# Performance work log

Measured on AMD Instinct MI355X. Metric: run time of the kernel, lower is better.

The kernel has to match this reference:

```python
import jax, jax.numpy as jnp
import numpy as np

B, S, D_MODEL, H, D_K, D_V = 2, 2048, 1024, 16, 64, 64


def setup_inputs() -> dict:
    key = jax.random.key(0)
    ks = jax.random.split(key, 12)
    s = 0.02
    inp = {
        "Q": jax.random.normal(ks[0], (B, S, D_MODEL), jnp.float32),
        "K": jax.random.normal(ks[1], (B, S, D_MODEL), jnp.float32),
        "V": jax.random.normal(ks[2], (B, S, D_MODEL), jnp.float32),
        # causal 0/1 mask, broadcastable to [B, H, S, S]
        "mask": jnp.tril(jnp.ones((S, S), jnp.int32))[None, None, :, :],
        "Wq": jax.random.normal(ks[3], (D_MODEL, H * D_K), jnp.float32) * s,
        "bq": jnp.zeros((H * D_K,), jnp.float32),
        "Wk": jax.random.normal(ks[4], (D_MODEL, H * D_K), jnp.float32) * s,
        "bk": jnp.zeros((H * D_K,), jnp.float32),
        "Wv": jax.random.normal(ks[5], (D_MODEL, H * D_V), jnp.float32) * s,
        "bv": jnp.zeros((H * D_V,), jnp.float32),
        "Wo": jax.random.normal(ks[6], (H * D_V, D_MODEL), jnp.float32) * s,
        "bo": jnp.zeros((D_MODEL,), jnp.float32),
    }
    return inp


def reference(Q, K, V, mask, Wq, bq, Wk, bk, Wv, bv, Wo, bo):
    b = Q.shape[0]
    # project and split heads: [B, S, H*dk] -> [B, H, S, dk]
    q = (Q @ Wq + bq).reshape(b, -1, H, D_K).transpose(0, 2, 1, 3)
    k = (K @ Wk + bk).reshape(b, -1, H, D_K).transpose(0, 2, 1, 3)
    v = (V @ Wv + bv).reshape(b, -1, H, D_V).transpose(0, 2, 1, 3)
    scale = 1.0 / np.sqrt(D_K).astype(np.float32)
    scores = jnp.einsum("bhqd,bhkd->bhqk", q, k) * scale
    scores = jnp.where(mask == 0, jnp.float32(-1e9), scores)
    attn = jax.nn.softmax(scores, axis=-1)
    context = jnp.einsum("bhqk,bhkd->bhqd", attn, v)
    context = context.transpose(0, 2, 1, 3).reshape(b, -1, H * D_V)
    output = context @ Wo + bo  # dropout is identity in eval
    return output, attn
```

## Files before the change

### kernel.cpp

```cpp
#include <hip/hip_runtime.h>
#include <math.h>

#define S_LEN 2048
#define DMODEL 1024
#define NHEAD 16
#define HD 64
#define NBATCH 2

using short8  = __attribute__((ext_vector_type(8))) short;
using ushort8 = __attribute__((ext_vector_type(8))) unsigned short;
using floatx4 = __attribute__((ext_vector_type(4))) float;

__device__ __forceinline__ unsigned short f2b(float f) {
    unsigned int u = __float_as_uint(f);
    unsigned int r = (u + 0x7FFFu + ((u >> 16) & 1u)) >> 16;
    return (unsigned short)r;
}
__device__ __forceinline__ unsigned short f2bf(float f) {
    return (unsigned short)((__float_as_uint(f) + 0x8000u) >> 16);
}
__device__ __forceinline__ float b2f(unsigned short b) {
    return __uint_as_float(((unsigned int)b) << 16);
}

__device__ __forceinline__ void gll16(const void* g, void* l) {
    __builtin_amdgcn_global_load_lds(
        (const __attribute__((address_space(1))) unsigned int*)g,
        (__attribute__((address_space(3))) unsigned int*)l, 16, 0, 0);
}

#define C2_SCALE 0.18033688011112042f

__global__ __launch_bounds__(256)
void convert_bf16(const float* __restrict__ S0, const float* __restrict__ S1,
                  const float* __restrict__ S2,
                  unsigned short* __restrict__ D0, unsigned short* __restrict__ D1,
                  unsigned short* __restrict__ D2, int n4)
{
    const float* src = (blockIdx.z == 0) ? S0 : (blockIdx.z == 1) ? S1 : S2;
    unsigned short* dst = (blockIdx.z == 0) ? D0 : (blockIdx.z == 1) ? D1 : D2;
    int i = blockIdx.x * 256 + threadIdx.x;
    if (i < n4) {
        float4 v = ((const float4*)src)[i];
        ushort4 o;
        o.x = f2b(v.x); o.y = f2b(v.y); o.z = f2b(v.z); o.w = f2b(v.w);
        ((ushort4*)dst)[i] = o;
    }
}

__global__ __launch_bounds__(256)
void transpose_w(const float* __restrict__ W0, const float* __restrict__ W1,
                 const float* __restrict__ W2, const float* __restrict__ W3,
                 unsigned short* __restrict__ T0, unsigned short* __restrict__ T1,
                 unsigned short* __restrict__ T2, unsigned short* __restrict__ T3,
                 const float* __restrict__ bq, float* __restrict__ bqs)
{
    __shared__ float t[64][65];
    const float* W; unsigned short* T;
    switch (blockIdx.z) {
        case 0: W = W0; T = T0; break;
        case 1: W = W1; T = T1; break;
        case 2: W = W2; T = T2; break;
        default: W = W3; T = T3; break;
    }
    const int tid = threadIdx.x;
    const int c0 = blockIdx.x * 64;
    const int r0 = blockIdx.y * 64;

    if (blockIdx.z == 0 && blockIdx.x == 0 && blockIdx.y == 0) {
        float4 b4 = *(const float4*)(bq + tid * 4);
        b4.x *= C2_SCALE; b4.y *= C2_SCALE; b4.z *= C2_SCALE; b4.w *= C2_SCALE;
        *(float4*)(bqs + tid * 4) = b4;
    }

    const float scl = (blockIdx.z == 0) ? C2_SCALE : 1.0f;

    #pragma unroll
    for (int i = 0; i < 4; ++i) {
        int c = tid + i * 256;
        int r = c >> 4, off = (c & 15) * 4;
        float4 v = *(const float4*)(W + (size_t)(r0 + r) * DMODEL + c0 + off);
        t[r][off + 0] = v.x; t[r][off + 1] = v.y;
        t[r][off + 2] = v.z; t[r][off + 3] = v.w;
    }
    __syncthreads();
    #pragma unroll
    for (int i = 0; i < 4; ++i) {
        int c = tid + i * 256;
        int n = c >> 4, off = (c & 15) * 4;
        ushort4 o;
        o.x = f2b(t[off + 0][n] * scl); o.y = f2b(t[off + 1][n] * scl);
        o.z = f2b(t[off + 2][n] * scl); o.w = f2b(t[off + 3][n] * scl);
        *(ushort4*)(T + (size_t)(c0 + n) * DMODEL + r0 + off) = o;
    }
}

__global__ __launch_bounds__(256)
void gemm_qkv(const unsigned short* __restrict__ X0, const unsigned short* __restrict__ X1,
              const unsigned short* __restrict__ X2,
              const unsigned short* __restrict__ W0, const unsigned short* __restrict__ W1,
              const unsigned short* __restrict__ W2,
              const float* __restrict__ b0, const float* __restrict__ b1,
              const float* __restrict__ b2,
              unsigned short* __restrict__ o0, unsigned short* __restrict__ o1,
              unsigned short* __restrict__ o2)
{
    __shared__ unsigned short Xs[128 * 64];
    __shared__ unsigned short Ws[128 * 64];

    const unsigned short* X  = (blockIdx.z == 0) ? X0 : (blockIdx.z == 1) ? X1 : X2;
    const unsigned short* Wt = (blockIdx.z == 0) ? W0 : (blockIdx.z == 1) ? W1 : W2;
    const float* bias        = (blockIdx.z == 0) ? b0 : (blockIdx.z == 1) ? b1 : b2;
    unsigned short* outp     = (blockIdx.z == 0) ? o0 : (blockIdx.z == 1) ? o1 : o2;

    const int tid = threadIdx.x;
    const int lane = tid & 63, w = tid >> 6;
    const int l15 = lane & 15, l4 = lane >> 4;
    const int wr = w >> 1, wc = w & 1;
    const int row0 = blockIdx.y * 128;
    const int col0 = blockIdx.x * 128;

    const int srow = lane >> 3;
    const int sblk = (lane & 7) ^ srow;

    floatx4 acc[4][4] = {};

    for (int k0 = 0; k0 < DMODEL; k0 += 64) {
        __syncthreads();
        #pragma unroll
        for (int i = 0; i < 4; ++i)
            gll16(X + (size_t)(row0 + w * 32 + i * 8 + srow) * DMODEL + k0 + sblk * 8,
                  &Xs[(w * 32 + i * 8) * 64]);
        #pragma unroll
        for (int i = 0; i < 4; ++i)
            gll16(Wt + (size_t)(col0 + w * 32 + i * 8 + srow) * DMODEL + k0 + sblk * 8,
                  &Ws[(w * 32 + i * 8) * 64]);
        asm volatile("s_waitcnt vmcnt(0)" ::: "memory");
        __syncthreads();

        #pragma unroll
        for (int ks = 0; ks < 2; ++ks) {
            short8 a[4], b[4];
            #pragma unroll
            for (int m = 0; m < 4; ++m) {
                const int r = wr * 64 + m * 16 + l15;
                a[m] = *(const short8*)&Xs[r * 64 + (((ks * 4 + l4) ^ (r & 7)) << 3)];
            }
            #pragma unroll
            for (int n = 0; n < 4; ++n) {
                const int r = wc * 64 + n * 16 + l15;
                b[n] = *(const short8*)&Ws[r * 64 + (((ks * 4 + l4) ^ (r & 7)) << 3)];
            }
            #pragma unroll
            for (int m = 0; m < 4; ++m)
                #pragma unroll
                for (int n = 0; n < 4; ++n)
                    acc[m][n] = __builtin_amdgcn_mfma_f32_16x16x32_bf16(
                        a[m], b[n], acc[m][n], 0, 0, 0);
        }
    }

    float bl[4];
    #pragma unroll
    for (int n = 0; n < 4; ++n)
        bl[n] = bias[col0 + wc * 64 + n * 16 + l15];

    if (blockIdx.z != 2) {
        #pragma unroll
        for (int m = 0; m < 4; ++m)
            #pragma unroll
            for (int n = 0; n < 4; ++n) {
                const int gc = col0 + wc * 64 + n * 16 + l15;
                const int h = gc >> 6, d = gc & 63;
                #pragma unroll
                for (int reg = 0; reg < 4; ++reg) {
                    const int gr = row0 + wr * 64 + m * 16 + l4 * 4 + reg;
                    const int bb = gr >> 11, s = gr & 2047;
                    outp[(((size_t)bb * NHEAD + h) * S_LEN + s) * HD + d] =
                        f2b(acc[m][n][reg] + bl[n]);
                }
            }
    } else {
        #pragma unroll
        for (int m = 0; m < 4; ++m)
            #pragma unroll
            for (int n = 0; n < 4; ++n) {
                const int gc = col0 + wc * 64 + n * 16 + l15;
                const int h = gc >> 6, d = gc & 63;
                const int s0 = row0 + wr * 64 + m * 16 + l4 * 4;
                const int bb = s0 >> 11, sr = s0 & 2047;
                ushort4 pk;
                pk.x = f2b(acc[m][n][0] + bl[n]);
                pk.y = f2b(acc[m][n][1] + bl[n]);
                pk.z = f2b(acc[m][n][2] + bl[n]);
                pk.w = f2b(acc[m][n][3] + bl[n]);
                *(ushort4*)(outp + (((size_t)bb * NHEAD + h) * HD + d) * S_LEN + sr) = pk;
            }
    }
}

__global__ __launch_bounds__(256)
void gemm_out(const unsigned short* __restrict__ X, const unsigned short* __restrict__ Wt,
              const float* __restrict__ bias, float* __restrict__ out)
{
    __shared__ unsigned short Xs[128 * 64];
    __shared__ unsigned short Ws[64 * 64];

    const int tid = threadIdx.x;
    const int lane = tid & 63, w = tid >> 6;
    const int l15 = lane & 15, l4 = lane >> 4;
    const int wr = w >> 1, wc = w & 1;
    const int row0 = blockIdx.y * 128;
    const int col0 = blockIdx.x * 64;

    const int srow = lane >> 3;
    const int sblk = (lane & 7) ^ srow;

    floatx4 acc[4][2] = {};

    for (int k0 = 0; k0 < DMODEL; k0 += 64) {
        __syncthreads();
        #pragma unroll
        for (int i = 0; i < 4; ++i)
            gll16(X + (size_t)(row0 + w * 32 + i * 8 + srow) * DMODEL + k0 + sblk * 8,
                  &Xs[(w * 32 + i * 8) * 64]);
        #pragma unroll
        for (int i = 0; i < 2; ++i)
            gll16(Wt + (size_t)(col0 + w * 16 + i * 8 + srow) * DMODEL + k0 + sblk * 8,
                  &Ws[(w * 16 + i * 8) * 64]);
        asm volatile("s_waitcnt vmcnt(0)" ::: "memory");
        __syncthreads();

        #pragma unroll
        for (int ks = 0; ks < 2; ++ks) {
            short8 a[4], b[2];
            #pragma unroll
            for (int m = 0; m < 4; ++m) {
                const int r = wr * 64 + m * 16 + l15;
                a[m] = *(const short8*)&Xs[r * 64 + (((ks * 4 + l4) ^ (r & 7)) << 3)];
            }
            #pragma unroll
            for (int n = 0; n < 2; ++n) {
                const int r = wc * 32 + n * 16 + l15;
                b[n] = *(const short8*)&Ws[r * 64 + (((ks * 4 + l4) ^ (r & 7)) << 3)];
            }
            #pragma unroll
            for (int m = 0; m < 4; ++m)
                #pragma unroll
                for (int n = 0; n < 2; ++n)
                    acc[m][n] = __builtin_amdgcn_mfma_f32_16x16x32_bf16(
                        a[m], b[n], acc[m][n], 0, 0, 0);
        }
    }

    float bl[2];
    #pragma unroll
    for (int n = 0; n < 2; ++n)
        bl[n] = bias[col0 + wc * 32 + n * 16 + l15];

    #pragma unroll
    for (int m = 0; m < 4; ++m)
        #pragma unroll
        for (int n = 0; n < 2; ++n) {
            const int gc = col0 + wc * 32 + n * 16 + l15;
            #pragma unroll
            for (int reg = 0; reg < 4; ++reg) {
                const int gr = row0 + wr * 64 + m * 16 + l4 * 4 + reg;
                out[(size_t)gr * DMODEL + gc] = acc[m][n][reg] + bl[n];
            }
        }
}

__global__ __launch_bounds__(256)
void attn_mfma(const unsigned short* __restrict__ qg, const unsigned short* __restrict__ kg,
               const unsigned short* __restrict__ vtg, float* __restrict__ attn,
               unsigned short* __restrict__ ctx)
{
    __shared__ unsigned short Ks[2 * 64 * 64];
    __shared__ unsigned short Vt[64 * 64];
    __shared__ unsigned short Ps[64 * 88];

    const int tid = threadIdx.x;
    const int lane = tid & 63, w = tid >> 6;
    const int l15 = lane & 15, l4 = lane >> 4;

    const int i0 = blockIdx.x;
    const int local = i0 >> 3;
    const int bh = (i0 & 7) * 4 + (local & 3);
    const int qx = local >> 2;
    const int qb = (bh & 1) ? (31 - qx) : qx;
    const int row0 = qb * 64;

    const int srow = lane >> 3;
    const int sblk = (lane & 7) ^ srow;

    const unsigned short* qh = qg + (size_t)bh * S_LEN * HD;
    const unsigned short* kh = kg + (size_t)bh * S_LEN * HD;
    const unsigned short* vth = vtg + (size_t)bh * HD * S_LEN;
    float* attnh = attn + (size_t)bh * S_LEN * S_LEN;

    short8 qa[2];
    #pragma unroll
    for (int ks = 0; ks < 2; ++ks)
        qa[ks] = *(const short8*)(qh + (size_t)(row0 + w * 16 + l15) * HD + ks * 32 + l4 * 8);

    const int nt = qb + 1;

    #pragma unroll
    for (int i = 0; i < 2; ++i)
        gll16(kh + (size_t)(w * 16 + i * 8 + srow) * HD + sblk * 8,
              &Ks[(w * 16 + i * 8) * 64]);

    float lsum[4] = {};
    for (int jt = 0; jt < nt; ++jt) {
        const int cur = jt & 1;
        __builtin_amdgcn_s_barrier();
        if (jt + 1 < nt) {
            #pragma unroll
            for (int i = 0; i < 2; ++i)
                gll16(kh + (size_t)((jt + 1) * 64 + w * 16 + i * 8 + srow) * HD + sblk * 8,
                      &Ks[(cur ^ 1) * 4096 + (w * 16 + i * 8) * 64]);
            asm volatile("s_waitcnt vmcnt(2)" ::: "memory");
        } else {
            asm volatile("s_waitcnt vmcnt(0)" ::: "memory");
        }
        __builtin_amdgcn_s_barrier();

        floatx4 sf[4] = {};
        #pragma unroll
        for (int ks = 0; ks < 2; ++ks) {
            short8 kb[4];
            #pragma unroll
            for (int c = 0; c < 4; ++c) {
                const int r = c * 16 + l15;
                kb[c] = *(const short8*)&Ks[cur * 4096 + r * 64
                                            + (((ks * 4 + l4) ^ (r & 7)) << 3)];
            }
            #pragma unroll
            for (int c = 0; c < 4; ++c)
                sf[c] = __builtin_amdgcn_mfma_f32_16x16x32_bf16(qa[ks], kb[c], sf[c], 0, 0, 0);
        }

        const int rbase = row0 + w * 16;
        if (jt * 64 + 63 <= rbase) {
            #pragma unroll
            for (int c = 0; c < 4; ++c)
                #pragma unroll
                for (int reg = 0; reg < 4; ++reg)
                    lsum[reg] += exp2f(sf[c][reg]);
        } else {
            #pragma unroll
            for (int c = 0; c < 4; ++c) {
                const int jcol = jt * 64 + c * 16 + l15;
                #pragma unroll
                for (int reg = 0; reg < 4; ++reg) {
                    const int grow = rbase + l4 * 4 + reg;
                    lsum[reg] += (jcol <= grow) ? exp2f(sf[c][reg]) : 0.f;
                }
            }
        }
    }

    float nl2[4];
    #pragma unroll
    for (int reg = 0; reg < 4; ++reg) {
        float s = lsum[reg];
        #pragma unroll
        for (int off = 1; off < 16; off <<= 1)
            s += __shfl_xor(s, off);
        nl2[reg] = -__log2f(s);
    }

    asm volatile("s_waitcnt vmcnt(0) lgkmcnt(0)" ::: "memory");
    __builtin_amdgcn_s_barrier();
    #pragma unroll
    for (int i = 0; i < 2; ++i)
        gll16(kh + (size_t)(w * 16 + i * 8 + srow) * HD + sblk * 8,
              &Ks[(w * 16 + i * 8) * 64]);

    floatx4 o[4] = {};
    for (int jt = 0; jt < nt; ++jt) {
        const int buf = jt & 1;
        if (jt <= 1) {
            asm volatile("s_waitcnt vmcnt(0)" ::: "memory");
        } else {
            asm volatile("s_waitcnt vmcnt(4)" ::: "memory");
        }
        __builtin_amdgcn_s_barrier();

        #pragma unroll
        for (int i = 0; i < 2; ++i)
            gll16(vth + (size_t)(w * 16 + i * 8 + srow) * S_LEN + jt * 64 + sblk * 8,
                  &Vt[(w * 16 + i * 8) * 64]);
        if (jt + 1 < nt) {
            #pragma unroll
            for (int i = 0; i < 2; ++i)
                gll16(kh + (size_t)((jt + 1) * 64 + w * 16 + i * 8 + srow) * HD + sblk * 8,
                      &Ks[(buf ^ 1) * 4096 + (w * 16 + i * 8) * 64]);
        }

        if (jt >= 1) {
            #pragma unroll
            for (int i2 = 0; i2 < 4; ++i2) {
                const int idx = lane + i2 * 64;
                const int r = w * 16 + (idx >> 4), c4 = (idx & 15) * 4;
                const ushort4 pb = *(const ushort4*)&Ps[r * 88 + c4];
                floatx4 pf;
                pf[0] = b2f(pb.x); pf[1] = b2f(pb.y); pf[2] = b2f(pb.z); pf[3] = b2f(pb.w);
                __builtin_nontemporal_store(
                    pf, (floatx4*)(attnh + (size_t)(row0 + r) * S_LEN + (jt - 1) * 64 + c4));
            }
        }

        floatx4 sf[4] = {};
        #pragma unroll
        for (int ks = 0; ks < 2; ++ks) {
            short8 kb[4];
            #pragma unroll
            for (int c = 0; c < 4; ++c) {
                const int r = c * 16 + l15;
                kb[c] = *(const short8*)&Ks[buf * 4096 + r * 64
                                            + (((ks * 4 + l4) ^ (r & 7)) << 3)];
            }
            #pragma unroll
            for (int c = 0; c < 4; ++c)
                sf[c] = __builtin_amdgcn_mfma_f32_16x16x32_bf16(qa[ks], kb[c], sf[c], 0, 0, 0);
        }

        const int rbase = row0 + w * 16;
        const bool full = (jt * 64 + 63 <= rbase);
        #pragma unroll
        for (int c = 0; c < 4; ++c) {
            const int jcol = jt * 64 + c * 16 + l15;
            #pragma unroll
            for (int reg = 0; reg < 4; ++reg) {
                const int rl = w * 16 + l4 * 4 + reg;
                float p = exp2f(sf[c][reg] + nl2[reg]);
                if (!full && jcol > rbase + l4 * 4 + reg) p = 0.f;
                Ps[rl * 88 + c * 16 + l15] = f2bf(p);
            }
        }
        if (jt + 1 < nt) {
            if (jt == 0) {
                asm volatile("s_waitcnt vmcnt(2) lgkmcnt(0)" ::: "memory");
            } else {
                asm volatile("s_waitcnt vmcnt(6) lgkmcnt(0)" ::: "memory");
            }
        } else {
            if (jt == 0) {
                asm volatile("s_waitcnt vmcnt(0) lgkmcnt(0)" ::: "memory");
            } else {
                asm volatile("s_waitcnt vmcnt(4) lgkmcnt(0)" ::: "memory");
            }
        }
        __builtin_amdgcn_s_barrier();

        #pragma unroll
        for (int ks = 0; ks < 2; ++ks) {
            const short8 pa = *(const short8*)&Ps[(w * 16 + l15) * 88 + ks * 32 + l4 * 8];
            #pragma unroll
            for (int c = 0; c < 4; ++c) {
                const int r = c * 16 + l15;
                const short8 vb = *(const short8*)&Vt[r * 64
                                                     + (((ks * 4 + l4) ^ (r & 7)) << 3)];
                o[c] = __builtin_amdgcn_mfma_f32_16x16x32_bf16(pa, vb, o[c], 0, 0, 0);
            }
        }
    }

    {
        const int jt = nt - 1;
        #pragma unroll
        for (int i2 = 0; i2 < 4; ++i2) {
            const int idx = lane + i2 * 64;
            const int r = w * 16 + (idx >> 4), c4 = (idx & 15) * 4;
            const ushort4 pb = *(const ushort4*)&Ps[r * 88 + c4];
            floatx4 pf;
            pf[0] = b2f(pb.x); pf[1] = b2f(pb.y); pf[2] = b2f(pb.z); pf[3] = b2f(pb.w);
            __builtin_nontemporal_store(
                pf, (floatx4*)(attnh + (size_t)(row0 + r) * S_LEN + jt * 64 + c4));
        }
    }

    const int b = bh >> 4, h = bh & 15;
    #pragma unroll
    for (int c = 0; c < 4; ++c)
        #pragma unroll
        for (int reg = 0; reg < 4; ++reg) {
            const int gr = row0 + w * 16 + l4 * 4 + reg;
            const int d = c * 16 + l15;
            ctx[((size_t)b * S_LEN + gr) * DMODEL + h * HD + d] = f2b(o[c][reg]);
        }

    const floatx4 z4 = {0.f, 0.f, 0.f, 0.f};
    for (int jt = nt; jt < S_LEN / 64; ++jt) {
        #pragma unroll
        for (int i = 0; i < 4; ++i) {
            const int idx = tid + i * 256;
            const int r = idx >> 4, off = (idx & 15) * 4;
            __builtin_nontemporal_store(
                z4, (floatx4*)(attnh + (size_t)(row0 + r) * S_LEN + jt * 64 + off));
        }
    }
}

extern "C" void kernel_launch(void* const* d_in, const int* in_sizes, int n_in,
                              void* d_out, int out_size, void* d_ws, size_t ws_size,
                              hipStream_t stream)
{
    const float* Q  = (const float*)d_in[0];
    const float* K  = (const float*)d_in[1];
    const float* V  = (const float*)d_in[2];
    const float* Wq = (const float*)d_in[4];
    const float* bq = (const float*)d_in[5];
    const float* Wk = (const float*)d_in[6];
    const float* bk = (const float*)d_in[7];
    const float* Wv = (const float*)d_in[8];
    const float* bv = (const float*)d_in[9];
    const float* Wo = (const float*)d_in[10];
    const float* bo = (const float*)d_in[11];

    float* out  = (float*)d_out;
    float* attn = out + (size_t)NBATCH * S_LEN * DMODEL;

    const size_t per = (size_t)NBATCH * S_LEN * DMODEL;
    const size_t wsz = (size_t)DMODEL * DMODEL;
    unsigned short* Xq  = (unsigned short*)d_ws;
    unsigned short* Xk  = Xq + per;
    unsigned short* Xv  = Xk + per;
    unsigned short* Wtq = Xv + per;
    unsigned short* Wtk = Wtq + wsz;
    unsigned short* Wtv = Wtk + wsz;
    unsigned short* Wto = Wtv + wsz;
    unsigned short* qhw = Wto + wsz;
    unsigned short* khw = qhw + per;
    unsigned short* vhw = khw + per;
    unsigned short* ctx = vhw + per;
    float* bqs = (float*)(ctx + per);

    const int n4 = (int)(per / 4);
    convert_bf16<<<dim3((n4 + 255) / 256, 1, 3), 256, 0, stream>>>(
        Q, K, V, Xq, Xk, Xv, n4);
    transpose_w<<<dim3(16, 16, 4), 256, 0, stream>>>(
        Wq, Wk, Wv, Wo, Wtq, Wtk, Wtv, Wto, bq, bqs);

    gemm_qkv<<<dim3(DMODEL / 128, (NBATCH * S_LEN) / 128, 3), 256, 0, stream>>>(
        Xq, Xk, Xv, Wtq, Wtk, Wtv, bqs, bk, bv, qhw, khw, vhw);

    attn_mfma<<<1024, 256, 0, stream>>>(qhw, khw, vhw, attn, ctx);

    gemm_out<<<dim3(DMODEL / 64, (NBATCH * S_LEN) / 128), 256, 0, stream>>>(
        ctx, Wto, bo, out);
}
```

Measured before the change: 224.5 us.

## Enlarge attention query tile to 128 rows with 512-thread blocks

Each attention block now covers 128 query rows using 8 waves instead of 64 rows with 4 waves, so each K and V tile loaded into shared memory is reused by twice as many query rows. Per-wave async load counts and the matching s_waitcnt thresholds are adjusted, and fully masked key tiles are skipped in the row-sum pass. The aim is to cut redundant K/V global traffic and halve the block count. In exchange, blocks are bigger with more shared memory, there are fewer blocks for the CUs, and causal load imbalance may get worse while the kernel stays dominated by the attention-matrix writes.

```diff
diff --git a/kernel.cpp b/kernel.cpp
--- a/kernel.cpp
+++ b/kernel.cpp
@@ -271,14 +271,14 @@
         }
 }
 
-__global__ __launch_bounds__(256)
+__global__ __launch_bounds__(512)
 void attn_mfma(const unsigned short* __restrict__ qg, const unsigned short* __restrict__ kg,
                const unsigned short* __restrict__ vtg, float* __restrict__ attn,
                unsigned short* __restrict__ ctx)
 {
     __shared__ unsigned short Ks[2 * 64 * 64];
     __shared__ unsigned short Vt[64 * 64];
-    __shared__ unsigned short Ps[64 * 88];
+    __shared__ unsigned short Ps[128 * 88];
 
     const int tid = threadIdx.x;
     const int lane = tid & 63, w = tid >> 6;
@@ -288,8 +288,8 @@
     const int local = i0 >> 3;
     const int bh = (i0 & 7) * 4 + (local & 3);
     const int qx = local >> 2;
-    const int qb = (bh & 1) ? (31 - qx) : qx;
-    const int row0 = qb * 64;
+    const int qb = (bh & 1) ? (15 - qx) : qx;
+    const int row0 = qb * 128;
 
     const int srow = lane >> 3;
     const int sblk = (lane & 7) ^ srow;
@@ -304,23 +304,18 @@
     for (int ks = 0; ks < 2; ++ks)
         qa[ks] = *(const short8*)(qh + (size_t)(row0 + w * 16 + l15) * HD + ks * 32 + l4 * 8);
 
-    const int nt = qb + 1;
-
-    #pragma unroll
-    for (int i = 0; i < 2; ++i)
-        gll16(kh + (size_t)(w * 16 + i * 8 + srow) * HD + sblk * 8,
-              &Ks[(w * 16 + i * 8) * 64]);
+    const int nt = 2 * qb + 2;
+
+    gll16(kh + (size_t)(w * 8 + srow) * HD + sblk * 8, &Ks[(w * 8) * 64]);
 
     float lsum[4] = {};
     for (int jt = 0; jt < nt; ++jt) {
         const int cur = jt & 1;
         __builtin_amdgcn_s_barrier();
         if (jt + 1 < nt) {
-            #pragma unroll
-            for (int i = 0; i < 2; ++i)
-                gll16(kh + (size_t)((jt + 1) * 64 + w * 16 + i * 8 + srow) * HD + sblk * 8,
-                      &Ks[(cur ^ 1) * 4096 + (w * 16 + i * 8) * 64]);
-            asm volatile("s_waitcnt vmcnt(2)" ::: "memory");
+            gll16(kh + (size_t)((jt + 1) * 64 + w * 8 + srow) * HD + sblk * 8,
+                  &Ks[(cur ^ 1) * 4096 + (w * 8) * 64]);
+            asm volatile("s_waitcnt vmcnt(1)" ::: "memory");
         } else {
             asm volatile("s_waitcnt vmcnt(0)" ::: "memory");
         }
@@ -348,6 +343,7 @@
                 #pragma unroll
                 for (int reg = 0; reg < 4; ++reg)
                     lsum[reg] += exp2f(sf[c][reg]);
+        } else if (jt * 64 > rbase + 15) {
         } else {
             #pragma unroll
             for (int c = 0; c < 4; ++c) {
@@ -373,10 +369,7 @@
 
     asm volatile("s_waitcnt vmcnt(0) lgkmcnt(0)" ::: "memory");
     __builtin_amdgcn_s_barrier();
-    #pragma unroll
-    for (int i = 0; i < 2; ++i)
-        gll16(kh + (size_t)(w * 16 + i * 8 + srow) * HD + sblk * 8,
-              &Ks[(w * 16 + i * 8) * 64]);
+    gll16(kh + (size_t)(w * 8 + srow) * HD + sblk * 8, &Ks[(w * 8) * 64]);
 
     floatx4 o[4] = {};
     for (int jt = 0; jt < nt; ++jt) {
@@ -388,15 +381,11 @@
         }
         __builtin_amdgcn_s_barrier();
 
-        #pragma unroll
-        for (int i = 0; i < 2; ++i)
-            gll16(vth + (size_t)(w * 16 + i * 8 + srow) * S_LEN + jt * 64 + sblk * 8,
-                  &Vt[(w * 16 + i * 8) * 64]);
+        gll16(vth + (size_t)(w * 8 + srow) * S_LEN + jt * 64 + sblk * 8,
+              &Vt[(w * 8) * 64]);
         if (jt + 1 < nt) {
-            #pragma unroll
-            for (int i = 0; i < 2; ++i)
-                gll16(kh + (size_t)((jt + 1) * 64 + w * 16 + i * 8 + srow) * HD + sblk * 8,
-                      &Ks[(buf ^ 1) * 4096 + (w * 16 + i * 8) * 64]);
+            gll16(kh + (size_t)((jt + 1) * 64 + w * 8 + srow) * HD + sblk * 8,
+                  &Ks[(buf ^ 1) * 4096 + (w * 8) * 64]);
         }
 
         if (jt >= 1) {
@@ -440,18 +429,13 @@
                 Ps[rl * 88 + c * 16 + l15] = f2bf(p);
             }
         }
-        if (jt + 1 < nt) {
-            if (jt == 0) {
-                asm volatile("s_waitcnt vmcnt(2) lgkmcnt(0)" ::: "memory");
-            } else {
-                asm volatile("s_waitcnt vmcnt(6) lgkmcnt(0)" ::: "memory");
-            }
+        if (jt == 0) {
+            if (nt > 1) { asm volatile("s_waitcnt vmcnt(1) lgkmcnt(0)" ::: "memory"); }
+            else        { asm volatile("s_waitcnt vmcnt(0) lgkmcnt(0)" ::: "memory"); }
+        } else if (jt + 1 < nt) {
+            asm volatile("s_waitcnt vmcnt(5) lgkmcnt(0)" ::: "memory");
         } else {
-            if (jt == 0) {
-                asm volatile("s_waitcnt vmcnt(0) lgkmcnt(0)" ::: "memory");
-            } else {
-                asm volatile("s_waitcnt vmcnt(4) lgkmcnt(0)" ::: "memory");
-            }
+            asm volatile("s_waitcnt vmcnt(4) lgkmcnt(0)" ::: "memory");
         }
         __builtin_amdgcn_s_barrier();
 
@@ -496,7 +480,7 @@
     for (int jt = nt; jt < S_LEN / 64; ++jt) {
         #pragma unroll
         for (int i = 0; i < 4; ++i) {
-            const int idx = tid + i * 256;
+            const int idx = tid + i * 512;
             const int r = idx >> 4, off = (idx & 15) * 4;
             __builtin_nontemporal_store(
                 z4, (floatx4*)(attnh + (size_t)(row0 + r) * S_LEN + jt * 64 + off));
@@ -547,7 +531,7 @@
     gemm_qkv<<<dim3(DMODEL / 128, (NBATCH * S_LEN) / 128, 3), 256, 0, stream>>>(
         Xq, Xk, Xv, Wtq, Wtk, Wtv, bqs, bk, bv, qhw, khw, vhw);
 
-    attn_mfma<<<1024, 256, 0, stream>>>(qhw, khw, vhw, attn, ctx);
+    attn_mfma<<<512, 512, 0, stream>>>(qhw, khw, vhw, attn, ctx);
 
     gemm_out<<<dim3(DMODEL / 64, (NBATCH * S_LEN) / 128), 256, 0, stream>>>(
         ctx, Wto, bo, out);
```

Result: slower. 237.7 us (+5.9%).
